# Performance work log

Hardware: AMD Instinct MI355X
Metric: run time of the kernel (lower is better)

## Reference

```python
import jax, jax.numpy as jnp
import numpy as np

N_ENS = 10   # LSTMs per ensemble
N_OPP = 5    # opponents
H_GEN = 10   # gen LSTM hidden
H_OPP = 5    # opp LSTM hidden


def setup_inputs() -> dict:
    key = jax.random.key(0)
    ks = iter(jax.random.split(key, 32))
    r = lambda shape, s=0.1: jax.random.normal(next(ks), shape, dtype=jnp.float32) * s
    return {
        "x": jax.random.normal(next(ks), (1, 1, 37), dtype=jnp.float32),
        # 10 gen LSTMs (input 12, hidden 10), stacked; torch gate order i,f,g,o
        "W_ih_gen": r((N_ENS, 4 * H_GEN, 12)),
        "W_hh_gen": r((N_ENS, 4 * H_GEN, H_GEN)),
        "b_ih_gen": r((N_ENS, 4 * H_GEN)),
        "b_hh_gen": r((N_ENS, 4 * H_GEN)),
        "h0_gen": r((N_ENS, H_GEN)),
        "c0_gen": r((N_ENS, H_GEN)),
        # 10 opp-game LSTMs (input 4, hidden 5), shared weights across opponents
        "W_ih_game": r((N_ENS, 4 * H_OPP, 4)),
        "W_hh_game": r((N_ENS, 4 * H_OPP, H_OPP)),
        "b_ih_game": r((N_ENS, 4 * H_OPP)),
        "b_hh_game": r((N_ENS, 4 * H_OPP)),
        # per-opponent, per-ensemble-member hidden/cell states
        "h0_game": r((N_OPP, N_ENS, H_OPP)),
        "c0_game": r((N_OPP, N_ENS, H_OPP)),
        # decision MLP
        "W1": r((50, 200)), "b1": r((50,)),
        "W2": r((10, 50)), "b2": r((10,)),
        "W3": r((1, 10)), "b3": r((1,)),
    }


def reference(x, W_ih_gen, W_hh_gen, b_ih_gen, b_hh_gen, h0_gen, c0_gen,
              W_ih_game, W_hh_game, b_ih_game, b_hh_game, h0_game, c0_game,
              W1, b1, W2, b2, W3, b3):
    xv = x[0, 0]  # seq_len = batch = 1 is forced by the 200-feature reshape

    # --- gen ensemble: 10 independent LSTM cells batched as one GEMM ---
    x_gen = xv[:12]
    g = (jnp.einsum('khi,i->kh', W_ih_gen, x_gen)
         + jnp.einsum('khj,kj->kh', W_hh_gen, h0_gen)
         + b_ih_gen + b_hh_gen)                      # [10, 40]
    ig, fg, gg, og = jnp.split(g, 4, axis=-1)
    c_gen = jax.nn.sigmoid(fg) * c0_gen + jax.nn.sigmoid(ig) * jnp.tanh(gg)
    h_gen = jax.nn.sigmoid(og) * jnp.tanh(c_gen)      # [10, 10]
    x_gen_out = h_gen.reshape(-1)                     # [100]

    # --- opponent game ensembles: 5 opps x 10 LSTMs batched ---
    x_opp = xv[12:].reshape(N_OPP, 5)
    active = x_opp[:, 0]
    xin = x_opp[:, 1:]                                # [5, 4]
    g2 = (jnp.einsum('khi,oi->okh', W_ih_game, xin)
          + jnp.einsum('khj,okj->okh', W_hh_game, h0_game)
          + b_ih_game + b_hh_game)                    # [5, 10, 20]
    i2, f2, g2g, o2 = jnp.split(g2, 4, axis=-1)
    c_game = jax.nn.sigmoid(f2) * c0_game + jax.nn.sigmoid(i2) * jnp.tanh(g2g)
    h_game = jax.nn.sigmoid(o2) * jnp.tanh(c_game)    # [5, 10, 5]

    # Source bug preserved: the 'round' loop concatenates x_opp_game (output of
    # the LAST game LSTM, i=9) ten more times; round-LSTM outputs never reach
    # the model output, so they are omitted here.
    feat = jnp.concatenate(
        [h_game.reshape(N_OPP, -1),                     # 10*5 = 50
         jnp.tile(h_game[:, -1, :], (1, N_ENS))],       # 10*5 = 50 (repeated)
        axis=1)                                         # [5, 100]

    # if int(x_active) == 1 -> truncation toward zero then equality with 1
    mask = (jnp.trunc(active) == 1).astype(feat.dtype)  # [5]
    cnt = mask.sum()
    avg = jnp.where(cnt > 0,
                    (mask[:, None] * feat).sum(0) / jnp.maximum(cnt, 1.0),
                    jnp.zeros((100,), feat.dtype))       # [100]

    h1 = jnp.tanh(jnp.concatenate([x_gen_out, avg]) @ W1.T + b1)
    h2 = jnp.tanh(h1 @ W2.T + b2)
    out = jnp.tanh(h2 @ W3.T + b3)
    return out.reshape(1, 1, 1)
```

## Files before the change

kernel.cpp:

```cpp
#include <hip/hip_runtime.h>

__device__ __forceinline__ float sigf(float x) { return 1.0f / (1.0f + expf(-x)); }

__global__ __launch_bounds__(384) void net6max_kernel(
    const float* __restrict__ x,
    const float* __restrict__ W_ih_gen, const float* __restrict__ W_hh_gen,
    const float* __restrict__ b_ih_gen, const float* __restrict__ b_hh_gen,
    const float* __restrict__ h0_gen,  const float* __restrict__ c0_gen,
    const float* __restrict__ W_ih_game, const float* __restrict__ W_hh_game,
    const float* __restrict__ b_ih_game, const float* __restrict__ b_hh_game,
    const float* __restrict__ h0_game, const float* __restrict__ c0_game,
    const float* __restrict__ W1, const float* __restrict__ b1,
    const float* __restrict__ W2, const float* __restrict__ b2,
    const float* __restrict__ W3, const float* __restrict__ b3,
    float* __restrict__ out)
{
    __shared__ float hg[100];
    __shared__ float hgame[250];
    __shared__ float avg_s[100];
    __shared__ float h1v[52];

    const int tid = threadIdx.x;

    float w1r[50];
    float b1r = 0.f;
    if (tid < 200) {
        const int row = tid >> 2, seg = tid & 3;
        const float* w = W1 + row * 200 + seg * 50;
        #pragma unroll
        for (int c = 0; c < 50; ++c) w1r[c] = w[c];
        if (seg == 0) b1r = b1[row];
    }
    float w2r[50];
    float b2r = 0.f, w3r = 0.f, b3r = 0.f;
    if (tid < 10) {
        const float* w = W2 + tid * 50;
        #pragma unroll
        for (int c = 0; c < 50; ++c) w2r[c] = w[c];
        b2r = b2[tid];
        w3r = W3[tid];
    }
    if (tid == 0) b3r = b3[0];

    if (tid < 100) {
        const int k = tid / 10, j = tid % 10;
        float acc[4];
        #pragma unroll
        for (int g = 0; g < 4; ++g) {
            const int r = k * 40 + g * 10 + j;
            float s = b_ih_gen[r] + b_hh_gen[r];
            const float* wi = W_ih_gen + r * 12;
            #pragma unroll
            for (int i = 0; i < 12; ++i) s += wi[i] * x[i];
            const float* wh = W_hh_gen + r * 10;
            const float* h0 = h0_gen + k * 10;
            #pragma unroll
            for (int jj = 0; jj < 10; ++jj) s += wh[jj] * h0[jj];
            acc[g] = s;
        }
        const float c = sigf(acc[1]) * c0_gen[tid] + sigf(acc[0]) * tanhf(acc[2]);
        hg[tid] = sigf(acc[3]) * tanhf(c);
    }
    if (tid >= 128 && tid < 378) {
        const int e = tid - 128;
        const int o = e / 50, rem = e % 50, k = rem / 5, j = rem % 5;
        float acc[4];
        #pragma unroll
        for (int g = 0; g < 4; ++g) {
            const int r = k * 20 + g * 5 + j;
            float s = b_ih_game[r] + b_hh_game[r];
            const float* wi = W_ih_game + r * 4;
            const float* xi = x + 12 + o * 5 + 1;
            #pragma unroll
            for (int i = 0; i < 4; ++i) s += wi[i] * xi[i];
            const float* wh = W_hh_game + r * 5;
            const float* h0 = h0_game + (o * 10 + k) * 5;
            #pragma unroll
            for (int jj = 0; jj < 5; ++jj) s += wh[jj] * h0[jj];
            acc[g] = s;
        }
        const float c = sigf(acc[1]) * c0_game[e] + sigf(acc[0]) * tanhf(acc[2]);
        hgame[e] = sigf(acc[3]) * tanhf(c);
    }
    __syncthreads();

    if (tid < 100) {
        float cnt = 0.f, s = 0.f;
        #pragma unroll
        for (int o = 0; o < 5; ++o) {
            const float m = (truncf(x[12 + o * 5]) == 1.0f) ? 1.0f : 0.0f;
            cnt += m;
            const float f = (tid < 50) ? hgame[o * 50 + tid]
                                       : hgame[o * 50 + 45 + (tid - 50) % 5];
            s += m * f;
        }
        avg_s[tid] = (cnt > 0.f) ? (s / cnt) : 0.f;
    }
    __syncthreads();

    if (tid < 200) {
        const int row = tid >> 2, seg = tid & 3;
        const float* v = (seg < 2) ? (hg + seg * 50) : (avg_s + (seg - 2) * 50);
        float p = 0.f;
        #pragma unroll
        for (int c = 0; c < 50; ++c) p += w1r[c] * v[c];
        p += __shfl_down(p, 2);
        p += __shfl_down(p, 1);
        if (seg == 0) h1v[row] = tanhf(p + b1r);
    }
    __syncthreads();

    if (tid < 64) {
        float h2 = 0.f;
        if (tid < 10) {
            float s = b2r;
            #pragma unroll
            for (int c = 0; c < 50; ++c) s += w2r[c] * h1v[c];
            h2 = tanhf(s);
        }
        float p = (tid < 10) ? w3r * h2 : 0.f;
        p += __shfl_xor(p, 8);
        p += __shfl_xor(p, 4);
        p += __shfl_xor(p, 2);
        p += __shfl_xor(p, 1);
        if (tid == 0) out[0] = tanhf(p + b3r);
    }
}

extern "C" void kernel_launch(void* const* d_in, const int* in_sizes, int n_in,
                              void* d_out, int out_size, void* d_ws, size_t ws_size,
                              hipStream_t stream) {
    (void)in_sizes; (void)n_in; (void)out_size; (void)d_ws; (void)ws_size;
    net6max_kernel<<<1, 384, 0, stream>>>(
        (const float*)d_in[0],
        (const float*)d_in[1],
        (const float*)d_in[2],
        (const float*)d_in[3],
        (const float*)d_in[4],
        (const float*)d_in[5],
        (const float*)d_in[6],
        (const float*)d_in[7],
        (const float*)d_in[8],
        (const float*)d_in[9],
        (const float*)d_in[10],
        (const float*)d_in[11],
        (const float*)d_in[12],
        (const float*)d_in[13],
        (const float*)d_in[14],
        (const float*)d_in[15],
        (const float*)d_in[16],
        (const float*)d_in[17],
        (const float*)d_in[18],
        (float*)d_out);
}
```

Baseline: 12.19 us.

## Split LSTM gates across threads with shuffle combine and vectorize weight loads

Gate computations for both LSTM ensembles are spread over more threads: one gate per thread for the gen cells and two gates per thread for the game cells. Activations are exchanged with warp shuffles, and the block size grows from 384 to 512 threads. Weight and input loads switch to float4/float2 vector loads, and the MLP dot products read float2 from shared memory. The aim is a shorter serial dependency chain per thread, in exchange for more threads, more redundant activation evaluations, and alignment assumptions on the input pointers.

After: 11.29 us. -7.4%, faster.

```diff
diff --git a/kernel.cpp b/kernel.cpp
--- a/kernel.cpp
+++ b/kernel.cpp
@@ -2,7 +2,7 @@
 
 __device__ __forceinline__ float sigf(float x) { return 1.0f / (1.0f + expf(-x)); }
 
-__global__ __launch_bounds__(384) void net6max_kernel(
+__global__ __launch_bounds__(512) void net6max_kernel(
     const float* __restrict__ x,
     const float* __restrict__ W_ih_gen, const float* __restrict__ W_hh_gen,
     const float* __restrict__ b_ih_gen, const float* __restrict__ b_hh_gen,
@@ -15,72 +15,96 @@
     const float* __restrict__ W3, const float* __restrict__ b3,
     float* __restrict__ out)
 {
-    __shared__ float hg[100];
-    __shared__ float hgame[250];
-    __shared__ float avg_s[100];
-    __shared__ float h1v[52];
+    __shared__ __align__(16) float hg[100];
+    __shared__ __align__(16) float hgame[250];
+    __shared__ __align__(16) float avg_s[100];
+    __shared__ __align__(16) float h1v[52];
 
     const int tid = threadIdx.x;
 
-    float w1r[50];
-    float b1r = 0.f;
+    float s_gen = 0.f, c0g = 0.f;
+    if (tid < 400) {
+        const int cell = tid >> 2, g = tid & 3;
+        const int k = cell / 10, j = cell % 10;
+        const int r = k * 40 + g * 10 + j;
+        const float4* wi4 = (const float4*)(W_ih_gen + r * 12);
+        const float4* x4  = (const float4*)x;
+        const float4 wa = wi4[0], wb = wi4[1], wc = wi4[2];
+        const float4 xa = x4[0],  xb = x4[1],  xc = x4[2];
+        float s = b_ih_gen[r] + b_hh_gen[r];
+        s += wa.x*xa.x + wa.y*xa.y + wa.z*xa.z + wa.w*xa.w;
+        s += wb.x*xb.x + wb.y*xb.y + wb.z*xb.z + wb.w*xb.w;
+        s += wc.x*xc.x + wc.y*xc.y + wc.z*xc.z + wc.w*xc.w;
+        const float2* wh2 = (const float2*)(W_hh_gen + r * 10);
+        const float2* h02 = (const float2*)(h0_gen + k * 10);
+        #pragma unroll
+        for (int q = 0; q < 5; ++q) {
+            const float2 w = wh2[q], h = h02[q];
+            s += w.x*h.x + w.y*h.y;
+        }
+        s_gen = s;
+        if (g == 0) c0g = c0_gen[cell];
+    }
+
+    float su = 0.f, sv = 0.f, c0gm = 0.f;
+    if (tid < 500) {
+        const int c2 = tid >> 1, half = tid & 1;
+        const int o = c2 / 50, rem = c2 % 50, k = rem / 5, j = rem % 5;
+        const float* xi = x + 12 + o * 5 + 1;
+        const float x0 = xi[0], x1 = xi[1], x2 = xi[2], x3 = xi[3];
+        const float* h0 = h0_game + (o * 10 + k) * 5;
+        const float h00 = h0[0], h01 = h0[1], h02v = h0[2], h03 = h0[3], h04 = h0[4];
+        #pragma unroll
+        for (int gg = 0; gg < 2; ++gg) {
+            const int g = half * 2 + gg;
+            const int r = k * 20 + g * 5 + j;
+            const float4 wi = *(const float4*)(W_ih_game + r * 4);
+            float s = b_ih_game[r] + b_hh_game[r];
+            s += wi.x*x0 + wi.y*x1 + wi.z*x2 + wi.w*x3;
+            const float* wh = W_hh_game + r * 5;
+            s += wh[0]*h00 + wh[1]*h01 + wh[2]*h02v + wh[3]*h03 + wh[4]*h04;
+            if (gg == 0) su = s; else sv = s;
+        }
+        if (half == 0) c0gm = c0_game[c2];
+    }
+
+    float2 w1r[25]; float b1r = 0.f;
     if (tid < 200) {
         const int row = tid >> 2, seg = tid & 3;
-        const float* w = W1 + row * 200 + seg * 50;
+        const float2* w = (const float2*)(W1 + row * 200 + seg * 50);
         #pragma unroll
-        for (int c = 0; c < 50; ++c) w1r[c] = w[c];
+        for (int q = 0; q < 25; ++q) w1r[q] = w[q];
         if (seg == 0) b1r = b1[row];
     }
-    float w2r[50];
-    float b2r = 0.f, w3r = 0.f, b3r = 0.f;
+    float2 w2r[25]; float b2r = 0.f, w3r = 0.f, b3r = 0.f;
     if (tid < 10) {
-        const float* w = W2 + tid * 50;
+        const float2* w = (const float2*)(W2 + tid * 50);
         #pragma unroll
-        for (int c = 0; c < 50; ++c) w2r[c] = w[c];
+        for (int q = 0; q < 25; ++q) w2r[q] = w[q];
         b2r = b2[tid];
         w3r = W3[tid];
     }
     if (tid == 0) b3r = b3[0];
 
-    if (tid < 100) {
-        const int k = tid / 10, j = tid % 10;
-        float acc[4];
-        #pragma unroll
-        for (int g = 0; g < 4; ++g) {
-            const int r = k * 40 + g * 10 + j;
-            float s = b_ih_gen[r] + b_hh_gen[r];
-            const float* wi = W_ih_gen + r * 12;
-            #pragma unroll
-            for (int i = 0; i < 12; ++i) s += wi[i] * x[i];
-            const float* wh = W_hh_gen + r * 10;
-            const float* h0 = h0_gen + k * 10;
-            #pragma unroll
-            for (int jj = 0; jj < 10; ++jj) s += wh[jj] * h0[jj];
-            acc[g] = s;
+    {
+        const float a  = ((tid & 3) == 2) ? tanhf(s_gen) : sigf(s_gen);
+        const float a1 = __shfl_xor(a, 1);
+        const float a2 = __shfl_xor(a, 2);
+        const float a3 = __shfl_xor(a, 3);
+        if (tid < 400 && (tid & 3) == 0) {
+            const float c = a1 * c0g + a * a2;
+            hg[tid >> 2] = a3 * tanhf(c);
         }
-        const float c = sigf(acc[1]) * c0_gen[tid] + sigf(acc[0]) * tanhf(acc[2]);
-        hg[tid] = sigf(acc[3]) * tanhf(c);
     }
-    if (tid >= 128 && tid < 378) {
-        const int e = tid - 128;
-        const int o = e / 50, rem = e % 50, k = rem / 5, j = rem % 5;
-        float acc[4];
-        #pragma unroll
-        for (int g = 0; g < 4; ++g) {
-            const int r = k * 20 + g * 5 + j;
-            float s = b_ih_game[r] + b_hh_game[r];
-            const float* wi = W_ih_game + r * 4;
-            const float* xi = x + 12 + o * 5 + 1;
-            #pragma unroll
-            for (int i = 0; i < 4; ++i) s += wi[i] * xi[i];
-            const float* wh = W_hh_game + r * 5;
-            const float* h0 = h0_game + (o * 10 + k) * 5;
-            #pragma unroll
-            for (int jj = 0; jj < 5; ++jj) s += wh[jj] * h0[jj];
-            acc[g] = s;
+    {
+        const float u = ((tid & 1) == 0) ? sigf(su) : tanhf(su);
+        const float v = sigf(sv);
+        const float up = __shfl_xor(u, 1);
+        const float vp = __shfl_xor(v, 1);
+        if (tid < 500 && (tid & 1) == 0) {
+            const float c = v * c0gm + u * up;
+            hgame[tid >> 1] = vp * tanhf(c);
         }
-        const float c = sigf(acc[1]) * c0_game[e] + sigf(acc[0]) * tanhf(acc[2]);
-        hgame[e] = sigf(acc[3]) * tanhf(c);
     }
     __syncthreads();
 
@@ -100,10 +124,11 @@
 
     if (tid < 200) {
         const int row = tid >> 2, seg = tid & 3;
-        const float* v = (seg < 2) ? (hg + seg * 50) : (avg_s + (seg - 2) * 50);
+        const float2* v2 = (seg < 2) ? (const float2*)(hg + seg * 50)
+                                     : (const float2*)(avg_s + (seg - 2) * 50);
         float p = 0.f;
         #pragma unroll
-        for (int c = 0; c < 50; ++c) p += w1r[c] * v[c];
+        for (int q = 0; q < 25; ++q) p += w1r[q].x * v2[q].x + w1r[q].y * v2[q].y;
         p += __shfl_down(p, 2);
         p += __shfl_down(p, 1);
         if (seg == 0) h1v[row] = tanhf(p + b1r);
@@ -114,8 +139,9 @@
         float h2 = 0.f;
         if (tid < 10) {
             float s = b2r;
+            const float2* h1v2 = (const float2*)h1v;
             #pragma unroll
-            for (int c = 0; c < 50; ++c) s += w2r[c] * h1v[c];
+            for (int q = 0; q < 25; ++q) s += w2r[q].x * h1v2[q].x + w2r[q].y * h1v2[q].y;
             h2 = tanhf(s);
         }
         float p = (tid < 10) ? w3r * h2 : 0.f;
@@ -131,7 +157,7 @@
                               void* d_out, int out_size, void* d_ws, size_t ws_size,
                               hipStream_t stream) {
     (void)in_sizes; (void)n_in; (void)out_size; (void)d_ws; (void)ws_size;
-    net6max_kernel<<<1, 384, 0, stream>>>(
+    net6max_kernel<<<1, 512, 0, stream>>>(
         (const float*)d_in[0],
         (const float*)d_in[1],
         (const float*)d_in[2],
```
